# Kernel tuning notes

Measured on AMD Instinct MI355X. Metric: run time of the kernel, lower is better.

Reference implementation:

```python
import jax, jax.numpy as jnp
import numpy as np

B, N, T, C = 16, 12, 128, 128  # batch, num_classes (nodes), temporal, channels


def _bn(x, gamma, beta, eps=1e-5):
    # BatchNorm2d in training mode: stats over (batch, t, c), channel axis 1, biased var
    mean = jnp.mean(x, axis=(0, 2, 3), keepdims=True)
    var = jnp.var(x, axis=(0, 2, 3), keepdims=True)
    xn = (x - mean) * jax.lax.rsqrt(var + eps)
    return xn * gamma[None, :, None, None] + beta[None, :, None, None]


def setup_inputs() -> dict:
    key = jax.random.key(0)
    ks = jax.random.split(key, 3)
    scale = np.float32(np.sqrt(2.0 / C))
    inp = {
        'x': jax.random.normal(ks[0], (B, N, T, C), dtype=jnp.float32),
        'edge': jax.random.normal(ks[1], (B, N * N, T, C), dtype=jnp.float32),
    }
    wk = jax.random.split(ks[2], 10)
    for name, k in zip(['A1', 'B1', 'E1', 'U1', 'V1', 'A2', 'B2', 'E2', 'U2', 'V2'], wk):
        inp[name] = jax.random.normal(k, (C, C), dtype=jnp.float32) * scale
    for name, dim in [('g_e1', N * N), ('b_e1', N * N), ('g_v1', N), ('b_v1', N),
                      ('g_e2', N * N), ('b_e2', N * N), ('g_v2', N), ('b_v2', N)]:
        inp[name] = jnp.ones((dim,), jnp.float32) if name[0] == 'g' else jnp.zeros((dim,), jnp.float32)
    return inp


def _forward(x, edge, A1, B1, E1, U1, V1, A2, B2, E2, U2, V2,
             g_e1, b_e1, g_v1, b_v1, g_e2, b_e2, g_v2, b_v2):
    # create_e_matrix: edge index e = i*N + j; 'end' selects node i, 'start' selects node j.
    # Dense incidence einsums become pure gathers; the transpose einsum is a
    # scatter-add over j, i.e. a reshape + sum.
    i_idx = jnp.repeat(jnp.arange(N), N)  # end-node of each edge
    j_idx = jnp.tile(jnp.arange(N), N)    # start-node of each edge
    b, _, t, c = x.shape

    def layer(x, edge, A, Bw, E, U, V, ge, be, gv, bv, mask_node):
        res = x
        edge_upd = (x @ A.T)[:, i_idx] + (x @ Bw.T)[:, j_idx] + edge @ E.T
        edge_upd = _bn(edge_upd, ge, be)
        edge_upd = jnp.where(jnp.isnan(edge_upd), 0.0, edge_upd)
        edge = edge + jax.nn.relu(edge_upd)
        e = jax.nn.sigmoid(edge)
        e = jax.nn.softmax(e.reshape(b, N, N, t, c), axis=2).reshape(b, N * N, t, c)
        Ujx = (x @ V.T)[:, j_idx]
        agg = (e * Ujx).reshape(b, N, N, t, c).sum(axis=2) / N  # scatter to end nodes
        xn = _bn(x @ U.T + agg, gv, bv)
        if mask_node:  # original only NaN-masks node BN in layer 1
            xn = jnp.where(jnp.isnan(xn), 0.0, xn)
        return jax.nn.relu(res + xn), edge

    x, edge = layer(x, edge, A1, B1, E1, U1, V1, g_e1, b_e1, g_v1, b_v1, True)
    x, edge = layer(x, edge, A2, B2, E2, U2, V2, g_e2, b_e2, g_v2, b_v2, False)
    return x, edge


def reference(x, edge, A1, B1, E1, U1, V1, A2, B2, E2, U2, V2,
              g_e1, b_e1, g_v1, b_v1, g_e2, b_e2, g_v2, b_v2):
    return _forward(x, edge, A1, B1, E1, U1, V1, A2, B2, E2, U2, V2,
                    g_e1, b_e1, g_v1, b_v1, g_e2, b_e2, g_v2, b_v2)
```

## Files before the change

kernel.cpp:

```cpp
#include <hip/hip_runtime.h>
#include <hip/hip_bf16.h>

#define BB 16
#define NN 12
#define NE 144
#define TT 128
#define CC 128

typedef __attribute__((ext_vector_type(8))) short v8s;
typedef __attribute__((ext_vector_type(4))) short v4s;
typedef __attribute__((ext_vector_type(4))) float v4f;

__device__ __forceinline__ short f2bf(float f) {
    unsigned u = __float_as_uint(f);
    u += 0x7fffu + ((u >> 16) & 1u);
    return (short)(u >> 16);
}
__device__ __forceinline__ float bf2f(unsigned short u) {
    return __uint_as_float(((unsigned)u) << 16);
}
__device__ __forceinline__ v4s f4_to_bf4(float4 a) {
    v4s r; r[0] = f2bf(a.x); r[1] = f2bf(a.y); r[2] = f2bf(a.z); r[3] = f2bf(a.w); return r;
}
__device__ __forceinline__ size_t ebfslot(int b, int e, int t) {
    return (((size_t)(b * NE + e) * TT) + t) * CC;
}

__global__ __launch_bounds__(256) void kW(
    const float* A1, const float* B1, const float* E1, const float* U1, const float* V1,
    const float* A2, const float* B2, const float* E2, const float* U2, const float* V2,
    unsigned short* wb)
{
    int idx = blockIdx.x * 256 + threadIdx.x;
    int w = idx >> 14, r = idx & 16383;
    const float* s;
    switch (w) {
        case 0: s = A1; break; case 1: s = B1; break; case 2: s = E1; break;
        case 3: s = U1; break; case 4: s = V1; break; case 5: s = A2; break;
        case 6: s = B2; break; case 7: s = E2; break; case 8: s = U2; break;
        default: s = V2; break;
    }
    wb[idx] = (unsigned short)f2bf(s[r]);
}

__global__ __launch_bounds__(256) void kP(
    const float* __restrict__ x, const unsigned short* __restrict__ wb,
    int sA, int sB, int sV, int sU,
    unsigned short* __restrict__ oA, unsigned short* __restrict__ oB,
    unsigned short* __restrict__ oV, unsigned short* __restrict__ oU)
{
    __shared__ unsigned short xt[64][136];
    int tid = threadIdx.x;
    int m0 = blockIdx.x * 64;
    #pragma unroll
    for (int it = 0; it < 8; ++it) {
        int f = it * 256 + tid;
        int row = f >> 5, c4 = f & 31;
        float4 v = *reinterpret_cast<const float4*>(x + (size_t)m0 * 128 + (size_t)f * 4);
        *reinterpret_cast<v4s*>(&xt[row][c4 * 4]) = f4_to_bf4(v);
    }
    __syncthreads();
    int lane = tid & 63, wid = tid >> 6;
    int l15 = lane & 15, l4 = lane >> 4;

    const unsigned short* Ws[4] = { wb + (size_t)sA * 16384, wb + (size_t)sB * 16384,
                                    wb + (size_t)sV * 16384, wb + (size_t)sU * 16384 };
    unsigned short* Os[4] = { oA, oB, oV, oU };

    #pragma unroll
    for (int w = 0; w < 4; ++w) {
        const unsigned short* W = Ws[w];
        unsigned short* out = Os[w];
        v8s bfr[2][4];
        #pragma unroll
        for (int nt2 = 0; nt2 < 2; ++nt2) {
            int col = (wid * 2 + nt2) * 16 + l15;
            #pragma unroll
            for (int kk = 0; kk < 4; ++kk)
                bfr[nt2][kk] = *reinterpret_cast<const v8s*>(W + col * 128 + kk * 32 + l4 * 8);
        }
        v4f acc[4][2] = {};
        #pragma unroll
        for (int kk = 0; kk < 4; ++kk) {
            #pragma unroll
            for (int mt = 0; mt < 4; ++mt) {
                v8s a = *reinterpret_cast<const v8s*>(&xt[mt * 16 + l15][kk * 32 + l4 * 8]);
                acc[mt][0] = __builtin_amdgcn_mfma_f32_16x16x32_bf16(a, bfr[0][kk], acc[mt][0], 0, 0, 0);
                acc[mt][1] = __builtin_amdgcn_mfma_f32_16x16x32_bf16(a, bfr[1][kk], acc[mt][1], 0, 0, 0);
            }
        }
        #pragma unroll
        for (int mt = 0; mt < 4; ++mt) {
            #pragma unroll
            for (int nt2 = 0; nt2 < 2; ++nt2) {
                int col = (wid * 2 + nt2) * 16 + l15;
                #pragma unroll
                for (int reg = 0; reg < 4; ++reg) {
                    int rowg = m0 + mt * 16 + l4 * 4 + reg;
                    out[(size_t)rowg * 128 + col] = (unsigned short)f2bf(acc[mt][nt2][reg]);
                }
            }
        }
    }
}

template<bool IN_F32>
__global__ __launch_bounds__(256) void kA(
    const float* __restrict__ ef32, const unsigned short* __restrict__ ebf_in,
    unsigned short* __restrict__ ebf_out,
    unsigned short* __restrict__ updg,
    const unsigned short* __restrict__ xA, const unsigned short* __restrict__ xB,
    const unsigned short* __restrict__ Ebf, float* __restrict__ epart)
{
    __shared__ unsigned short ebt[48][136];
    __shared__ unsigned short xab[16][136];
    __shared__ float srow[48], qrow[48];
    int tid = threadIdx.x;
    int bid = blockIdx.x;
    int third = bid % 3; int bt = bid / 3;
    int b = bt >> 7, t = bt & 127;
    if (tid < 48) { srow[tid] = 0.f; qrow[tid] = 0.f; }

    if constexpr (IN_F32) {
        const float* eb = ef32 + ebfslot(b, third * 48, t);
        #pragma unroll
        for (int it = 0; it < 6; ++it) {
            int f = it * 256 + tid;
            int row = f >> 5, c4 = f & 31;
            float4 v = *reinterpret_cast<const float4*>(eb + (size_t)row * (TT * CC) + c4 * 4);
            *reinterpret_cast<v4s*>(&ebt[row][c4 * 4]) = f4_to_bf4(v);
        }
    } else {
        #pragma unroll
        for (int it = 0; it < 3; ++it) {
            int f = it * 256 + tid;
            int row = f >> 4, c8 = f & 15;
            *reinterpret_cast<v8s*>(&ebt[row][c8 * 8]) =
                *reinterpret_cast<const v8s*>(ebf_in + ebfslot(b, third * 48 + row, t) + c8 * 8);
        }
    }
    {
        int row = tid >> 4, c8 = tid & 15;
        const unsigned short* src = (row < 4)
            ? (xA + (((size_t)(b * NN + third * 4 + row) * TT) + t) * CC)
            : (xB + (((size_t)(b * NN + (row - 4)) * TT) + t) * CC);
        *reinterpret_cast<v8s*>(&xab[row][c8 * 8]) = *reinterpret_cast<const v8s*>(src + c8 * 8);
    }
    __syncthreads();
    if constexpr (IN_F32) {
        #pragma unroll
        for (int it = 0; it < 3; ++it) {
            int f = it * 256 + tid;
            int row = f >> 4, c8 = f & 15;
            *reinterpret_cast<v8s*>(ebf_out + ebfslot(b, third * 48 + row, t) + c8 * 8) =
                *reinterpret_cast<const v8s*>(&ebt[row][c8 * 8]);
        }
    }
    int lane = tid & 63, wid = tid >> 6;
    int l15 = lane & 15, l4 = lane >> 4;
    v8s bfr[2][4];
    #pragma unroll
    for (int nt2 = 0; nt2 < 2; ++nt2) {
        int col = (wid * 2 + nt2) * 16 + l15;
        #pragma unroll
        for (int kk = 0; kk < 4; ++kk)
            bfr[nt2][kk] = *reinterpret_cast<const v8s*>(Ebf + col * 128 + kk * 32 + l4 * 8);
    }
    v4f acc[3][2] = {};
    #pragma unroll
    for (int kk = 0; kk < 4; ++kk) {
        #pragma unroll
        for (int mt = 0; mt < 3; ++mt) {
            v8s a = *reinterpret_cast<const v8s*>(&ebt[mt * 16 + l15][kk * 32 + l4 * 8]);
            acc[mt][0] = __builtin_amdgcn_mfma_f32_16x16x32_bf16(a, bfr[0][kk], acc[mt][0], 0, 0, 0);
            acc[mt][1] = __builtin_amdgcn_mfma_f32_16x16x32_bf16(a, bfr[1][kk], acc[mt][1], 0, 0, 0);
        }
    }
    __syncthreads();
    #pragma unroll
    for (int mt = 0; mt < 3; ++mt) {
        #pragma unroll
        for (int reg = 0; reg < 4; ++reg) {
            int r = mt * 16 + l4 * 4 + reg;
            int il = r / 12, jl = r - il * 12;
            float s = 0.f, q = 0.f;
            #pragma unroll
            for (int nt2 = 0; nt2 < 2; ++nt2) {
                int col = (wid * 2 + nt2) * 16 + l15;
                float v = acc[mt][nt2][reg] + bf2f(xab[il][col]) + bf2f(xab[4 + jl][col]);
                s += v; q += v * v;
                ebt[r][col] = (unsigned short)f2bf(v);
            }
            #pragma unroll
            for (int off = 1; off < 16; off <<= 1) { s += __shfl_xor(s, off); q += __shfl_xor(q, off); }
            if (l15 == 0) { atomicAdd(&srow[r], s); atomicAdd(&qrow[r], q); }
        }
    }
    __syncthreads();
    #pragma unroll
    for (int it = 0; it < 3; ++it) {
        int f = it * 256 + tid;
        int row = f >> 4, c8 = f & 15;
        *reinterpret_cast<v8s*>(updg + (size_t)bid * 6144 + (size_t)f * 8) =
            *reinterpret_cast<const v8s*>(&ebt[row][c8 * 8]);
    }
    if (tid < 48) {
        epart[(size_t)bid * 96 + tid * 2 + 0] = srow[tid];
        epart[(size_t)bid * 96 + tid * 2 + 1] = qrow[tid];
    }
}

__global__ __launch_bounds__(256) void kRede(
    const float* __restrict__ epart, const float* __restrict__ g,
    const float* __restrict__ be, float* __restrict__ estats)
{
    int e = blockIdx.x;
    int third = e / 48, le = e % 48;
    float s = 0.f, q = 0.f;
    for (int bt = threadIdx.x; bt < 2048; bt += 256) {
        const float* p = epart + ((size_t)(bt * 3 + third) * 96 + le * 2);
        s += p[0]; q += p[1];
    }
    __shared__ float ss[4], qq[4];
    #pragma unroll
    for (int off = 32; off >= 1; off >>= 1) { s += __shfl_down(s, off); q += __shfl_down(q, off); }
    int wid = threadIdx.x >> 6;
    if ((threadIdx.x & 63) == 0) { ss[wid] = s; qq[wid] = q; }
    __syncthreads();
    if (threadIdx.x == 0) {
        s = ss[0] + ss[1] + ss[2] + ss[3];
        q = qq[0] + qq[1] + qq[2] + qq[3];
        const float M = 262144.f;
        float mean = s / M;
        float var = q / M - mean * mean;
        float sc = g[e] * rsqrtf(var + 1e-5f);
        estats[e * 2] = sc;
        estats[e * 2 + 1] = be[e] - mean * sc;
    }
}

template<bool OUT_F32>
__global__ __launch_bounds__(256) void kC(
    const unsigned short* __restrict__ ebf,
    unsigned short* __restrict__ ebf_out,
    float* __restrict__ eout,
    const unsigned short* __restrict__ updg,
    const unsigned short* __restrict__ xV, const unsigned short* __restrict__ xU,
    const float* __restrict__ estats,
    unsigned short* __restrict__ yout, float* __restrict__ npart)
{
    __shared__ unsigned short se[48][136];
    __shared__ unsigned short xv[12][136];
    __shared__ float scs[48], shs[48];
    __shared__ float ns[4], nq[4];
    int tid = threadIdx.x;
    int bid = blockIdx.x;
    int third = bid % 3; int bt = bid / 3;
    int b = bt >> 7, t = bt & 127;
    if (tid < 48) { scs[tid] = estats[(third * 48 + tid) * 2]; shs[tid] = estats[(third * 48 + tid) * 2 + 1]; }
    if (tid < 4) { ns[tid] = 0.f; nq[tid] = 0.f; }
    if (tid < 192) {
        int row = tid >> 4, c8 = tid & 15;
        *reinterpret_cast<v8s*>(&xv[row][c8 * 8]) =
            *reinterpret_cast<const v8s*>(xV + (((size_t)(b * NN + row) * TT) + t) * CC + c8 * 8);
    }
    __syncthreads();
    #pragma unroll
    for (int it = 0; it < 3; ++it) {
        int f = it * 256 + tid;
        int row = f >> 4, c8 = f & 15;
        int eg = third * 48 + row;
        v8s uv = *reinterpret_cast<const v8s*>(updg + (size_t)bid * 6144 + (size_t)f * 8);
        size_t slot = ebfslot(b, eg, t) + c8 * 8;
        v8s evv = *reinterpret_cast<const v8s*>(ebf + slot);
        float sc = scs[row], sh = shs[row];
        float en[8];
        v8s nv;
        #pragma unroll
        for (int k = 0; k < 8; ++k) {
            en[k] = bf2f((unsigned short)evv[k]) + fmaxf(sc * bf2f((unsigned short)uv[k]) + sh, 0.f);
            nv[k] = f2bf(en[k]);
        }
        *reinterpret_cast<v8s*>(&se[row][c8 * 8]) = nv;
        if constexpr (OUT_F32) {
            size_t off = (((size_t)(b * NE + eg) * TT) + t) * CC + c8 * 8;
            *reinterpret_cast<float4*>(eout + off)     = make_float4(en[0], en[1], en[2], en[3]);
            *reinterpret_cast<float4*>(eout + off + 4) = make_float4(en[4], en[5], en[6], en[7]);
        } else {
            *reinterpret_cast<v8s*>(ebf_out + slot) = nv;
        }
    }
    __syncthreads();
    int lane = tid & 63;
    #pragma unroll
    for (int ph = 0; ph < 2; ++ph) {
        int unit = tid + ph * 256;
        int il = unit >> 7, c = unit & 127;
        float den = 0.f, ag = 0.f;
        #pragma unroll
        for (int j = 0; j < 12; ++j) {
            float sv = bf2f(se[il * 12 + j][c]);
            float sg = 1.f / (1.f + __expf(-sv));
            float ev = __expf(sg);
            den += ev;
            ag += ev * bf2f(xv[j][c]);
        }
        float agg = ag / (den * 12.f);
        int i = third * 4 + il;
        size_t xa = (((size_t)(b * NN + i) * TT) + t) * CC + c;
        float yv = bf2f(xU[xa]) + agg;
        unsigned short us = (unsigned short)f2bf(yv);
        yout[xa] = us;
        float yr = bf2f(us);
        float s1 = yr, s2 = yr * yr;
        #pragma unroll
        for (int off = 1; off < 64; off <<= 1) { s1 += __shfl_xor(s1, off); s2 += __shfl_xor(s2, off); }
        if (lane == 0) { atomicAdd(&ns[il], s1); atomicAdd(&nq[il], s2); }
    }
    __syncthreads();
    if (tid < 4) {
        npart[(size_t)bid * 8 + tid * 2 + 0] = ns[tid];
        npart[(size_t)bid * 8 + tid * 2 + 1] = nq[tid];
    }
}

__global__ __launch_bounds__(256) void kRedn(
    const float* __restrict__ npart, const float* __restrict__ g,
    const float* __restrict__ be, float* __restrict__ nstats)
{
    int n = blockIdx.x;
    int third = n >> 2, il = n & 3;
    float s = 0.f, q = 0.f;
    for (int bt = threadIdx.x; bt < 2048; bt += 256) {
        const float* p = npart + ((size_t)(bt * 3 + third) * 8 + il * 2);
        s += p[0]; q += p[1];
    }
    __shared__ float ss[4], qq[4];
    #pragma unroll
    for (int off = 32; off >= 1; off >>= 1) { s += __shfl_down(s, off); q += __shfl_down(q, off); }
    int wid = threadIdx.x >> 6;
    if ((threadIdx.x & 63) == 0) { ss[wid] = s; qq[wid] = q; }
    __syncthreads();
    if (threadIdx.x == 0) {
        s = ss[0] + ss[1] + ss[2] + ss[3];
        q = qq[0] + qq[1] + qq[2] + qq[3];
        const float M = 262144.f;
        float mean = s / M;
        float var = q / M - mean * mean;
        float sc = g[n] * rsqrtf(var + 1e-5f);
        nstats[n * 2] = sc;
        nstats[n * 2 + 1] = be[n] - mean * sc;
    }
}

__global__ __launch_bounds__(256) void kE(
    const float* xres, const unsigned short* __restrict__ yin,
    const float* __restrict__ nstats, float* xout)
{
    int idx4 = blockIdx.x * 256 + threadIdx.x;
    size_t base = (size_t)idx4 * 4;
    int n = (int)((base >> 14) % 12);
    float scv = nstats[n * 2], shv = nstats[n * 2 + 1];
    float4 xv = *reinterpret_cast<const float4*>(xres + base);
    v4s yv4 = *reinterpret_cast<const v4s*>(yin + base);
    float4 o;
    o.x = fmaxf(xv.x + scv * bf2f((unsigned short)yv4[0]) + shv, 0.f);
    o.y = fmaxf(xv.y + scv * bf2f((unsigned short)yv4[1]) + shv, 0.f);
    o.z = fmaxf(xv.z + scv * bf2f((unsigned short)yv4[2]) + shv, 0.f);
    o.w = fmaxf(xv.w + scv * bf2f((unsigned short)yv4[3]) + shv, 0.f);
    *reinterpret_cast<float4*>(xout + base) = o;
}

extern "C" void kernel_launch(void* const* d_in, const int* in_sizes, int n_in,
                              void* d_out, int out_size, void* d_ws, size_t ws_size,
                              hipStream_t stream)
{
    const float* x0 = (const float*)d_in[0];
    const float* e0 = (const float*)d_in[1];
    const float* W[10];
    for (int i = 0; i < 10; ++i) W[i] = (const float*)d_in[2 + i];
    const float* ge1 = (const float*)d_in[12];
    const float* be1 = (const float*)d_in[13];
    const float* gv1 = (const float*)d_in[14];
    const float* bv1 = (const float*)d_in[15];
    const float* ge2 = (const float*)d_in[16];
    const float* be2 = (const float*)d_in[17];
    const float* gv2 = (const float*)d_in[18];
    const float* bv2 = (const float*)d_in[19];

    const size_t SZX = (size_t)BB * NN * TT * CC;
    const size_t SZE = (size_t)BB * NE * TT * CC;
    float* out_x = (float*)d_out;
    float* out_e = out_x + SZX;

    unsigned short* ws16 = (unsigned short*)d_ws;
    unsigned short* xA = ws16;
    unsigned short* xB = ws16 + SZX;
    unsigned short* xV = ws16 + 2 * SZX;
    unsigned short* xU = ws16 + 3 * SZX;
    unsigned short* yb = ws16 + 4 * SZX;
    unsigned short* ebf = ws16 + 5 * SZX;
    unsigned short* upd = ebf + SZE;
    float* fpart  = (float*)(upd + SZE);
    float* epart  = fpart;
    float* estats = epart + 589824;
    float* npart  = estats + 288;
    float* nstats = npart + 49152;
    unsigned short* wb = (unsigned short*)(nstats + 24);

    float* x1 = out_x;

    kW<<<640, 256, 0, stream>>>(W[0], W[1], W[2], W[3], W[4], W[5], W[6], W[7], W[8], W[9], wb);

    kP<<<384, 256, 0, stream>>>(x0, wb, 0, 1, 4, 3, xA, xB, xV, xU);
    kA<true><<<6144, 256, 0, stream>>>(e0, nullptr, ebf, upd, xA, xB, wb + 2 * 16384, epart);
    kRede<<<144, 256, 0, stream>>>(epart, ge1, be1, estats);
    kC<false><<<6144, 256, 0, stream>>>(ebf, ebf, nullptr, upd, xV, xU, estats, yb, npart);
    kRedn<<<12, 256, 0, stream>>>(npart, gv1, bv1, nstats);
    kE<<<3072, 256, 0, stream>>>(x0, yb, nstats, x1);

    kP<<<384, 256, 0, stream>>>(x1, wb, 5, 6, 9, 8, xA, xB, xV, xU);
    kA<false><<<6144, 256, 0, stream>>>(nullptr, ebf, nullptr, upd, xA, xB, wb + 7 * 16384, epart);
    kRede<<<144, 256, 0, stream>>>(epart, ge2, be2, estats);
    kC<true><<<6144, 256, 0, stream>>>(ebf, nullptr, out_e, upd, xV, xU, estats, yb, npart);
    kRedn<<<12, 256, 0, stream>>>(npart, gv2, bv2, nstats);
    kE<<<3072, 256, 0, stream>>>(x1, yb, nstats, out_x);
}
```

Measured before the change: 309.8 us.

## Make edge-GEMM kernel persistent over time slices with direct register loads and identity-MFMA adds

The edge-update kernel now runs 768 blocks that each loop over 8 time steps, keeping the E weight fragments in registers and loading edge rows straight from global memory into MFMA operands instead of staging them through LDS. The xA/xB gather-adds are folded into the accumulators with MFMAs against an identity matrix. BN partial sums are kept in registers and reduced once per block. The update buffer is written in the MFMA fragment layout, so the consumer kernel reorders it through LDS and applies BN+ReLU there. This removes LDS traffic, barriers and per-block weight reloads, and shrinks the stats buffer, at the cost of fewer blocks and a non-coalesced fragment-layout update store.

New measurement: 365.1 us. 1.18x slower.

```diff
diff --git a/kernel.cpp b/kernel.cpp
--- a/kernel.cpp
+++ b/kernel.cpp
@@ -6,6 +6,7 @@
 #define NE 144
 #define TT 128
 #define CC 128
+#define T_PER 8
 
 typedef __attribute__((ext_vector_type(8))) short v8s;
 typedef __attribute__((ext_vector_type(4))) short v4s;
@@ -21,9 +22,6 @@
 }
 __device__ __forceinline__ v4s f4_to_bf4(float4 a) {
     v4s r; r[0] = f2bf(a.x); r[1] = f2bf(a.y); r[2] = f2bf(a.z); r[3] = f2bf(a.w); return r;
-}
-__device__ __forceinline__ size_t ebfslot(int b, int e, int t) {
-    return (((size_t)(b * NE + e) * TT) + t) * CC;
 }
 
 __global__ __launch_bounds__(256) void kW(
@@ -105,59 +103,22 @@
 }
 
 template<bool IN_F32>
-__global__ __launch_bounds__(256) void kA(
+__global__ __launch_bounds__(256, 3) void kA(
     const float* __restrict__ ef32, const unsigned short* __restrict__ ebf_in,
     unsigned short* __restrict__ ebf_out,
     unsigned short* __restrict__ updg,
-    const unsigned short* __restrict__ xA, const unsigned short* __restrict__ xB,
+    const unsigned short* __restrict__ xAp, const unsigned short* __restrict__ xBp,
     const unsigned short* __restrict__ Ebf, float* __restrict__ epart)
 {
-    __shared__ unsigned short ebt[48][136];
-    __shared__ unsigned short xab[16][136];
-    __shared__ float srow[48], qrow[48];
+    __shared__ float2 spart[48][4];
     int tid = threadIdx.x;
     int bid = blockIdx.x;
-    int third = bid % 3; int bt = bid / 3;
-    int b = bt >> 7, t = bt & 127;
-    if (tid < 48) { srow[tid] = 0.f; qrow[tid] = 0.f; }
-
-    if constexpr (IN_F32) {
-        const float* eb = ef32 + ebfslot(b, third * 48, t);
-        #pragma unroll
-        for (int it = 0; it < 6; ++it) {
-            int f = it * 256 + tid;
-            int row = f >> 5, c4 = f & 31;
-            float4 v = *reinterpret_cast<const float4*>(eb + (size_t)row * (TT * CC) + c4 * 4);
-            *reinterpret_cast<v4s*>(&ebt[row][c4 * 4]) = f4_to_bf4(v);
-        }
-    } else {
-        #pragma unroll
-        for (int it = 0; it < 3; ++it) {
-            int f = it * 256 + tid;
-            int row = f >> 4, c8 = f & 15;
-            *reinterpret_cast<v8s*>(&ebt[row][c8 * 8]) =
-                *reinterpret_cast<const v8s*>(ebf_in + ebfslot(b, third * 48 + row, t) + c8 * 8);
-        }
-    }
-    {
-        int row = tid >> 4, c8 = tid & 15;
-        const unsigned short* src = (row < 4)
-            ? (xA + (((size_t)(b * NN + third * 4 + row) * TT) + t) * CC)
-            : (xB + (((size_t)(b * NN + (row - 4)) * TT) + t) * CC);
-        *reinterpret_cast<v8s*>(&xab[row][c8 * 8]) = *reinterpret_cast<const v8s*>(src + c8 * 8);
-    }
-    __syncthreads();
-    if constexpr (IN_F32) {
-        #pragma unroll
-        for (int it = 0; it < 3; ++it) {
-            int f = it * 256 + tid;
-            int row = f >> 4, c8 = f & 15;
-            *reinterpret_cast<v8s*>(ebf_out + ebfslot(b, third * 48 + row, t) + c8 * 8) =
-                *reinterpret_cast<const v8s*>(&ebt[row][c8 * 8]);
-        }
-    }
+    int tg = bid & 15;
+    int q = bid >> 4;
+    int third = q % 3, b = q / 3;
     int lane = tid & 63, wid = tid >> 6;
     int l15 = lane & 15, l4 = lane >> 4;
+
     v8s bfr[2][4];
     #pragma unroll
     for (int nt2 = 0; nt2 < 2; ++nt2) {
@@ -166,47 +127,83 @@
         for (int kk = 0; kk < 4; ++kk)
             bfr[nt2][kk] = *reinterpret_cast<const v8s*>(Ebf + col * 128 + kk * 32 + l4 * 8);
     }
-    v4f acc[3][2] = {};
-    #pragma unroll
-    for (int kk = 0; kk < 4; ++kk) {
+    v8s idb;
+    #pragma unroll
+    for (int e = 0; e < 8; ++e)
+        idb[e] = (short)(((l4 * 8 + e) == l15) ? 0x3F80 : 0);
+
+    int rA0 = l15;
+    float sl[3][4] = {{0.f}}, ql[3][4] = {{0.f}};
+
+    #pragma unroll 2
+    for (int tt = 0; tt < T_PER; ++tt) {
+        int t = tg * T_PER + tt;
         #pragma unroll
         for (int mt = 0; mt < 3; ++mt) {
-            v8s a = *reinterpret_cast<const v8s*>(&ebt[mt * 16 + l15][kk * 32 + l4 * 8]);
-            acc[mt][0] = __builtin_amdgcn_mfma_f32_16x16x32_bf16(a, bfr[0][kk], acc[mt][0], 0, 0, 0);
-            acc[mt][1] = __builtin_amdgcn_mfma_f32_16x16x32_bf16(a, bfr[1][kk], acc[mt][1], 0, 0, 0);
-        }
-    }
-    __syncthreads();
+            v4f acc0 = {}, acc1 = {};
+            int rA = mt * 16 + rA0;
+            size_t erow = ((size_t)(b * NE + third * 48 + rA) * TT + t) * CC;
+            #pragma unroll
+            for (int kk = 0; kk < 4; ++kk) {
+                v8s a;
+                if constexpr (IN_F32) {
+                    const float* p = ef32 + erow + kk * 32 + l4 * 8;
+                    float4 f0 = *reinterpret_cast<const float4*>(p);
+                    float4 f1 = *reinterpret_cast<const float4*>(p + 4);
+                    a[0] = f2bf(f0.x); a[1] = f2bf(f0.y); a[2] = f2bf(f0.z); a[3] = f2bf(f0.w);
+                    a[4] = f2bf(f1.x); a[5] = f2bf(f1.y); a[6] = f2bf(f1.z); a[7] = f2bf(f1.w);
+                    *reinterpret_cast<v8s*>(ebf_out + erow + kk * 32 + l4 * 8) = a;
+                } else {
+                    a = *reinterpret_cast<const v8s*>(ebf_in + erow + kk * 32 + l4 * 8);
+                }
+                acc0 = __builtin_amdgcn_mfma_f32_16x16x32_bf16(a, bfr[0][kk], acc0, 0, 0, 0);
+                acc1 = __builtin_amdgcn_mfma_f32_16x16x32_bf16(a, bfr[1][kk], acc1, 0, 0, 0);
+            }
+            int iA = rA / 12, jA = rA - iA * 12;
+            size_t xarow = ((size_t)(b * NN + third * 4 + iA) * TT + t) * CC;
+            size_t xbrow = ((size_t)(b * NN + jA) * TT + t) * CC;
+            int cb0 = (wid * 2 + 0) * 16 + (l4 & 1) * 8;
+            int cb1 = (wid * 2 + 1) * 16 + (l4 & 1) * 8;
+            v8s a0 = *reinterpret_cast<const v8s*>(xAp + xarow + cb0);
+            v8s b0 = *reinterpret_cast<const v8s*>(xBp + xbrow + cb0);
+            v8s a1 = *reinterpret_cast<const v8s*>(xAp + xarow + cb1);
+            v8s b1 = *reinterpret_cast<const v8s*>(xBp + xbrow + cb1);
+            acc0 = __builtin_amdgcn_mfma_f32_16x16x32_bf16(a0, idb, acc0, 0, 0, 0);
+            acc0 = __builtin_amdgcn_mfma_f32_16x16x32_bf16(b0, idb, acc0, 0, 0, 0);
+            acc1 = __builtin_amdgcn_mfma_f32_16x16x32_bf16(a1, idb, acc1, 0, 0, 0);
+            acc1 = __builtin_amdgcn_mfma_f32_16x16x32_bf16(b1, idb, acc1, 0, 0, 0);
+
+            v8s up;
+            #pragma unroll
+            for (int k = 0; k < 8; ++k) {
+                float v = (k < 4) ? acc0[k] : acc1[k - 4];
+                sl[mt][k & 3] += v;
+                ql[mt][k & 3] += v * v;
+                up[k] = f2bf(v);
+            }
+            size_t unit = (size_t)q * TT + t;
+            *reinterpret_cast<v8s*>(updg + unit * 6144 + ((size_t)(mt * 256 + tid)) * 8) = up;
+        }
+    }
     #pragma unroll
     for (int mt = 0; mt < 3; ++mt) {
         #pragma unroll
         for (int reg = 0; reg < 4; ++reg) {
-            int r = mt * 16 + l4 * 4 + reg;
-            int il = r / 12, jl = r - il * 12;
-            float s = 0.f, q = 0.f;
-            #pragma unroll
-            for (int nt2 = 0; nt2 < 2; ++nt2) {
-                int col = (wid * 2 + nt2) * 16 + l15;
-                float v = acc[mt][nt2][reg] + bf2f(xab[il][col]) + bf2f(xab[4 + jl][col]);
-                s += v; q += v * v;
-                ebt[r][col] = (unsigned short)f2bf(v);
+            float s = sl[mt][reg], qv = ql[mt][reg];
+            #pragma unroll
+            for (int off = 1; off < 16; off <<= 1) {
+                s += __shfl_xor(s, off);
+                qv += __shfl_xor(qv, off);
             }
-            #pragma unroll
-            for (int off = 1; off < 16; off <<= 1) { s += __shfl_xor(s, off); q += __shfl_xor(q, off); }
-            if (l15 == 0) { atomicAdd(&srow[r], s); atomicAdd(&qrow[r], q); }
-        }
-    }
-    __syncthreads();
-    #pragma unroll
-    for (int it = 0; it < 3; ++it) {
-        int f = it * 256 + tid;
-        int row = f >> 4, c8 = f & 15;
-        *reinterpret_cast<v8s*>(updg + (size_t)bid * 6144 + (size_t)f * 8) =
-            *reinterpret_cast<const v8s*>(&ebt[row][c8 * 8]);
-    }
+            if (l15 == 0)
+                spart[mt * 16 + l4 * 4 + reg][wid] = make_float2(s, qv);
+        }
+    }
+    __syncthreads();
     if (tid < 48) {
-        epart[(size_t)bid * 96 + tid * 2 + 0] = srow[tid];
-        epart[(size_t)bid * 96 + tid * 2 + 1] = qrow[tid];
+        float2 a0 = spart[tid][0], a1 = spart[tid][1], a2 = spart[tid][2], a3 = spart[tid][3];
+        epart[(size_t)bid * 96 + tid * 2 + 0] = a0.x + a1.x + a2.x + a3.x;
+        epart[(size_t)bid * 96 + tid * 2 + 1] = a0.y + a1.y + a2.y + a3.y;
     }
 }
 
@@ -216,23 +213,23 @@
 {
     int e = blockIdx.x;
     int third = e / 48, le = e % 48;
-    float s = 0.f, q = 0.f;
-    for (int bt = threadIdx.x; bt < 2048; bt += 256) {
-        const float* p = epart + ((size_t)(bt * 3 + third) * 96 + le * 2);
-        s += p[0]; q += p[1];
-    }
+    int tid = threadIdx.x;
+    int b = tid >> 4, tg = tid & 15;
+    int bidA = b * 48 + third * 16 + tg;
+    float s = epart[(size_t)bidA * 96 + le * 2];
+    float qv = epart[(size_t)bidA * 96 + le * 2 + 1];
     __shared__ float ss[4], qq[4];
     #pragma unroll
-    for (int off = 32; off >= 1; off >>= 1) { s += __shfl_down(s, off); q += __shfl_down(q, off); }
-    int wid = threadIdx.x >> 6;
-    if ((threadIdx.x & 63) == 0) { ss[wid] = s; qq[wid] = q; }
-    __syncthreads();
-    if (threadIdx.x == 0) {
+    for (int off = 32; off >= 1; off >>= 1) { s += __shfl_down(s, off); qv += __shfl_down(qv, off); }
+    int wid = tid >> 6;
+    if ((tid & 63) == 0) { ss[wid] = s; qq[wid] = qv; }
+    __syncthreads();
+    if (tid == 0) {
         s = ss[0] + ss[1] + ss[2] + ss[3];
-        q = qq[0] + qq[1] + qq[2] + qq[3];
+        qv = qq[0] + qq[1] + qq[2] + qq[3];
         const float M = 262144.f;
         float mean = s / M;
-        float var = q / M - mean * mean;
+        float var = qv / M - mean * mean;
         float sc = g[e] * rsqrtf(var + 1e-5f);
         estats[e * 2] = sc;
         estats[e * 2 + 1] = be[e] - mean * sc;
@@ -241,23 +238,23 @@
 
 template<bool OUT_F32>
 __global__ __launch_bounds__(256) void kC(
-    const unsigned short* __restrict__ ebf,
-    unsigned short* __restrict__ ebf_out,
+    unsigned short* __restrict__ ebf,
     float* __restrict__ eout,
     const unsigned short* __restrict__ updg,
     const unsigned short* __restrict__ xV, const unsigned short* __restrict__ xU,
     const float* __restrict__ estats,
     unsigned short* __restrict__ yout, float* __restrict__ npart)
 {
-    __shared__ unsigned short se[48][136];
+    __shared__ unsigned short rb[48][136];
     __shared__ unsigned short xv[12][136];
-    __shared__ float scs[48], shs[48];
+    __shared__ float2 scf[48];
     __shared__ float ns[4], nq[4];
     int tid = threadIdx.x;
     int bid = blockIdx.x;
     int third = bid % 3; int bt = bid / 3;
     int b = bt >> 7, t = bt & 127;
-    if (tid < 48) { scs[tid] = estats[(third * 48 + tid) * 2]; shs[tid] = estats[(third * 48 + tid) * 2 + 1]; }
+    if (tid < 48) scf[tid] = make_float2(estats[(third * 48 + tid) * 2],
+                                         estats[(third * 48 + tid) * 2 + 1]);
     if (tid < 4) { ns[tid] = 0.f; nq[tid] = 0.f; }
     if (tid < 192) {
         int row = tid >> 4, c8 = tid & 15;
@@ -265,41 +262,54 @@
             *reinterpret_cast<const v8s*>(xV + (((size_t)(b * NN + row) * TT) + t) * CC + c8 * 8);
     }
     __syncthreads();
+    int lane = tid & 63, wid = tid >> 6;
+    int l15 = lane & 15, l4 = lane >> 4;
+    size_t unit = ((size_t)(b * 3 + third)) * TT + t;
+    const unsigned short* ub = updg + unit * 6144;
+    #pragma unroll
+    for (int mt = 0; mt < 3; ++mt) {
+        v8s uv = *reinterpret_cast<const v8s*>(ub + (size_t)(mt * 256 + tid) * 8);
+        #pragma unroll
+        for (int k = 0; k < 8; ++k) {
+            int r = mt * 16 + l4 * 4 + (k & 3);
+            int col = (wid * 2 + (k >> 2)) * 16 + l15;
+            float2 sc = scf[r];
+            float bn = fmaxf(sc.x * bf2f((unsigned short)uv[k]) + sc.y, 0.f);
+            rb[r][col] = (unsigned short)f2bf(bn);
+        }
+    }
+    __syncthreads();
     #pragma unroll
     for (int it = 0; it < 3; ++it) {
         int f = it * 256 + tid;
         int row = f >> 4, c8 = f & 15;
         int eg = third * 48 + row;
-        v8s uv = *reinterpret_cast<const v8s*>(updg + (size_t)bid * 6144 + (size_t)f * 8);
-        size_t slot = ebfslot(b, eg, t) + c8 * 8;
-        v8s evv = *reinterpret_cast<const v8s*>(ebf + slot);
-        float sc = scs[row], sh = shs[row];
-        float en[8];
-        v8s nv;
+        size_t goff = (((size_t)(b * NE + eg) * TT) + t) * CC + c8 * 8;
+        v8s rv = *reinterpret_cast<const v8s*>(&rb[row][c8 * 8]);
+        v8s ev = *reinterpret_cast<const v8s*>(ebf + goff);
+        float en[8]; v8s nv;
         #pragma unroll
         for (int k = 0; k < 8; ++k) {
-            en[k] = bf2f((unsigned short)evv[k]) + fmaxf(sc * bf2f((unsigned short)uv[k]) + sh, 0.f);
+            en[k] = bf2f((unsigned short)ev[k]) + bf2f((unsigned short)rv[k]);
             nv[k] = f2bf(en[k]);
         }
-        *reinterpret_cast<v8s*>(&se[row][c8 * 8]) = nv;
+        *reinterpret_cast<v8s*>(&rb[row][c8 * 8]) = nv;
         if constexpr (OUT_F32) {
-            size_t off = (((size_t)(b * NE + eg) * TT) + t) * CC + c8 * 8;
-            *reinterpret_cast<float4*>(eout + off)     = make_float4(en[0], en[1], en[2], en[3]);
-            *reinterpret_cast<float4*>(eout + off + 4) = make_float4(en[4], en[5], en[6], en[7]);
+            *reinterpret_cast<float4*>(eout + goff)     = make_float4(en[0], en[1], en[2], en[3]);
+            *reinterpret_cast<float4*>(eout + goff + 4) = make_float4(en[4], en[5], en[6], en[7]);
         } else {
-            *reinterpret_cast<v8s*>(ebf_out + slot) = nv;
-        }
-    }
-    __syncthreads();
-    int lane = tid & 63;
+            *reinterpret_cast<v8s*>(ebf + goff) = nv;
+        }
+    }
+    __syncthreads();
     #pragma unroll
     for (int ph = 0; ph < 2; ++ph) {
-        int unit = tid + ph * 256;
-        int il = unit >> 7, c = unit & 127;
+        int u = tid + ph * 256;
+        int il = u >> 7, c = u & 127;
         float den = 0.f, ag = 0.f;
         #pragma unroll
         for (int j = 0; j < 12; ++j) {
-            float sv = bf2f(se[il * 12 + j][c]);
+            float sv = bf2f(rb[il * 12 + j][c]);
             float sg = 1.f / (1.f + __expf(-sv));
             float ev = __expf(sg);
             den += ev;
@@ -361,13 +371,13 @@
     size_t base = (size_t)idx4 * 4;
     int n = (int)((base >> 14) % 12);
     float scv = nstats[n * 2], shv = nstats[n * 2 + 1];
-    float4 xv = *reinterpret_cast<const float4*>(xres + base);
+    float4 xvv = *reinterpret_cast<const float4*>(xres + base);
     v4s yv4 = *reinterpret_cast<const v4s*>(yin + base);
     float4 o;
-    o.x = fmaxf(xv.x + scv * bf2f((unsigned short)yv4[0]) + shv, 0.f);
-    o.y = fmaxf(xv.y + scv * bf2f((unsigned short)yv4[1]) + shv, 0.f);
-    o.z = fmaxf(xv.z + scv * bf2f((unsigned short)yv4[2]) + shv, 0.f);
-    o.w = fmaxf(xv.w + scv * bf2f((unsigned short)yv4[3]) + shv, 0.f);
+    o.x = fmaxf(xvv.x + scv * bf2f((unsigned short)yv4[0]) + shv, 0.f);
+    o.y = fmaxf(xvv.y + scv * bf2f((unsigned short)yv4[1]) + shv, 0.f);
+    o.z = fmaxf(xvv.z + scv * bf2f((unsigned short)yv4[2]) + shv, 0.f);
+    o.w = fmaxf(xvv.w + scv * bf2f((unsigned short)yv4[3]) + shv, 0.f);
     *reinterpret_cast<float4*>(xout + base) = o;
 }
 
@@ -401,9 +411,8 @@
     unsigned short* yb = ws16 + 4 * SZX;
     unsigned short* ebf = ws16 + 5 * SZX;
     unsigned short* upd = ebf + SZE;
-    float* fpart  = (float*)(upd + SZE);
-    float* epart  = fpart;
-    float* estats = epart + 589824;
+    float* epart  = (float*)(upd + SZE);
+    float* estats = epart + 73728;
     float* npart  = estats + 288;
     float* nstats = npart + 49152;
     unsigned short* wb = (unsigned short*)(nstats + 24);
@@ -413,16 +422,16 @@
     kW<<<640, 256, 0, stream>>>(W[0], W[1], W[2], W[3], W[4], W[5], W[6], W[7], W[8], W[9], wb);
 
     kP<<<384, 256, 0, stream>>>(x0, wb, 0, 1, 4, 3, xA, xB, xV, xU);
-    kA<true><<<6144, 256, 0, stream>>>(e0, nullptr, ebf, upd, xA, xB, wb + 2 * 16384, epart);
+    kA<true><<<768, 256, 0, stream>>>(e0, nullptr, ebf, upd, xA, xB, wb + 2 * 16384, epart);
     kRede<<<144, 256, 0, stream>>>(epart, ge1, be1, estats);
-    kC<false><<<6144, 256, 0, stream>>>(ebf, ebf, nullptr, upd, xV, xU, estats, yb, npart);
+    kC<false><<<6144, 256, 0, stream>>>(ebf, nullptr, upd, xV, xU, estats, yb, npart);
     kRedn<<<12, 256, 0, stream>>>(npart, gv1, bv1, nstats);
     kE<<<3072, 256, 0, stream>>>(x0, yb, nstats, x1);
 
     kP<<<384, 256, 0, stream>>>(x1, wb, 5, 6, 9, 8, xA, xB, xV, xU);
-    kA<false><<<6144, 256, 0, stream>>>(nullptr, ebf, nullptr, upd, xA, xB, wb + 7 * 16384, epart);
+    kA<false><<<768, 256, 0, stream>>>(nullptr, ebf, nullptr, upd, xA, xB, wb + 7 * 16384, epart);
     kRede<<<144, 256, 0, stream>>>(epart, ge2, be2, estats);
-    kC<true><<<6144, 256, 0, stream>>>(ebf, nullptr, out_e, upd, xV, xU, estats, yb, npart);
+    kC<true><<<6144, 256, 0, stream>>>(ebf, out_e, upd, xV, xU, estats, yb, npart);
     kRedn<<<12, 256, 0, stream>>>(npart, gv2, bv2, nstats);
     kE<<<3072, 256, 0, stream>>>(x1, yb, nstats, out_x);
 }
```
